# Optimization experiments

Measured on AMD Instinct MI355X. Metric: run time of the kernel, lower is better.

Reference implementation:

```python
import jax, jax.numpy as jnp
import numpy as np

NUM_HEADS = 16
D_MODEL = 1024
D_K = D_MODEL // NUM_HEADS


def setup_inputs() -> dict:
    key = jax.random.key(0)
    ks = jax.random.split(key, 11)
    B, S = 2, 2048
    s = 1.0 / np.sqrt(D_MODEL)
    return {
        "Q": jax.random.normal(ks[0], (B, S, D_MODEL), jnp.float32),
        "K": jax.random.normal(ks[1], (B, S, D_MODEL), jnp.float32),
        "V": jax.random.normal(ks[2], (B, S, D_MODEL), jnp.float32),
        "Wq": jax.random.normal(ks[3], (D_MODEL, D_MODEL), jnp.float32) * s,
        "bq": jnp.zeros((D_MODEL,), jnp.float32),
        "Wk": jax.random.normal(ks[4], (D_MODEL, D_MODEL), jnp.float32) * s,
        "bk": jnp.zeros((D_MODEL,), jnp.float32),
        "Wv": jax.random.normal(ks[5], (D_MODEL, D_MODEL), jnp.float32) * s,
        "bv": jnp.zeros((D_MODEL,), jnp.float32),
        "Wo": jax.random.normal(ks[6], (D_MODEL, D_MODEL), jnp.float32) * s,
        "bo": jnp.zeros((D_MODEL,), jnp.float32),
    }


def _split_heads(x):
    B, S, _ = x.shape
    return x.reshape(B, S, NUM_HEADS, D_K).transpose(0, 2, 1, 3)  # (B,H,S,Dk)


def reference(Q, K, V, Wq, bq, Wk, bk, Wv, bv, Wo, bo):
    q = _split_heads(Q @ Wq + bq)
    k = _split_heads(K @ Wk + bk)
    v = _split_heads(V @ Wv + bv)
    scores = jnp.einsum("bhqd,bhkd->bhqk", q, k) / jnp.sqrt(jnp.asarray(D_K, q.dtype))
    attn = jax.nn.softmax(scores, axis=-1)
    out = jnp.einsum("bhqk,bhkd->bhqd", attn, v)  # (B,H,S,Dk)
    B, H, S, Dk = out.shape
    combined = out.transpose(0, 2, 1, 3).reshape(B, S, H * Dk)
    return combined @ Wo + bo
```

## Files before the change

kernel.cpp:

```cpp
#include <hip/hip_runtime.h>
#include <stdint.h>

#define DM   1024
#define NH   16
#define DKH  64
#define SEQ  2048
#define NB   2

typedef __attribute__((ext_vector_type(8))) short  frag8;
typedef __attribute__((ext_vector_type(4))) short  frag4;
typedef __attribute__((ext_vector_type(4))) short  short4v;
typedef __attribute__((ext_vector_type(8))) short  short8v;
typedef __attribute__((ext_vector_type(4))) float  f32x4;

__device__ __forceinline__ unsigned short f2bf(float x){
  unsigned u = __float_as_uint(x);
  u += 0x7fffu + ((u >> 16) & 1u);
  return (unsigned short)(u >> 16);
}

__device__ __forceinline__ float dev_exp2(float x){
  return __builtin_amdgcn_exp2f(x);
}

#define GLOAD16(GP, LP) __builtin_amdgcn_global_load_lds( \
    (__attribute__((address_space(1))) void*)(GP), \
    (__attribute__((address_space(3))) void*)(LP), 16, 0, 0)

#define LDSFENCE() do{ asm volatile("" ::: "memory"); \
                       __builtin_amdgcn_sched_barrier(0); }while(0)


__global__ __launch_bounds__(256) void cast_qkv(const float* __restrict__ Q,
                                                const float* __restrict__ K,
                                                const float* __restrict__ V,
                                                short* __restrict__ dst){
  const int z = blockIdx.z;
  const float* src = (z == 0) ? Q : (z == 1 ? K : V);
  const int i = (blockIdx.x * 256 + threadIdx.x) * 4;
  float4 f = *(const float4*)(src + i);
  short4v s;
  s.x = (short)f2bf(f.x); s.y = (short)f2bf(f.y);
  s.z = (short)f2bf(f.z); s.w = (short)f2bf(f.w);
  *(short4v*)(dst + (long)z * (SEQ*NB*DM) + i) = s;
}

__global__ __launch_bounds__(256) void wtrans(const float* __restrict__ Wq,
                                              const float* __restrict__ Wk,
                                              const float* __restrict__ Wv,
                                              const float* __restrict__ Wo,
                                              short* __restrict__ wt){
  const int z = blockIdx.z;
  const float* W = (z == 0) ? Wq : (z == 1 ? Wk : (z == 2 ? Wv : Wo));
  short* out = wt + (long)z * (DM*DM);
  __shared__ float t[32][33];
  const int n0 = blockIdx.x * 32, k0 = blockIdx.y * 32;
  const int c = threadIdx.x & 31, r0 = threadIdx.x >> 5;
#pragma unroll
  for (int i = 0; i < 4; ++i){
    int r = r0 + i * 8;
    t[r][c] = W[(k0 + r) * DM + n0 + c];
  }
  __syncthreads();
#pragma unroll
  for (int i = 0; i < 4; ++i){
    int r = r0 + i * 8;
    out[(n0 + r) * DM + k0 + c] = (short)f2bf(t[c][r]);
  }
}

__device__ __forceinline__ void store_out(short* p, float v){ *p = (short)f2bf(v); }
__device__ __forceinline__ void store_out(float* p, float v){ *p = v; }

template<typename OT>
__global__ __launch_bounds__(256) void gemm_bt(const short* __restrict__ Abase, long Astride,
                                               const short* __restrict__ Btbase, long Btstride,
                                               const float* __restrict__ bias0,
                                               const float* __restrict__ bias1,
                                               const float* __restrict__ bias2,
                                               OT* __restrict__ Cbase, long Cstride,
                                               float qscale){
  const int z = blockIdx.z;
  const short* A  = Abase + (long)z * Astride;
  const short* Bt = Btbase + (long)z * Btstride;
  OT* C = Cbase + (long)z * Cstride;
  const float* bias = (z == 0) ? bias0 : (z == 1 ? bias1 : bias2);
  const float scale = (z == 0) ? qscale : 1.0f;
  const int KD = DM, ND = DM;

  __shared__ __align__(16) short As[128 * 64];
  __shared__ __align__(16) short Bs[128 * 64];

  const int tid = threadIdx.x;
  const int w = tid >> 6, lane = tid & 63, l15 = lane & 15, quad = lane >> 4;
  const int wy = w >> 1, wx = w & 1;
  const int bm = blockIdx.x * 128, bn = blockIdx.y * 128;
  const int lrow = lane >> 3;
  const int lcolsw = (((lane & 7) ^ lrow) & 7) * 8;

  f32x4 acc[4][4] = {};

  for (int kt = 0; kt < KD; kt += 64){
#pragma unroll
    for (int i = 0; i < 4; ++i){
      int j = w * 4 + i;
      GLOAD16(A  + (bm + j * 8 + lrow) * KD + kt + lcolsw, &As[j * 512]);
      GLOAD16(Bt + (bn + j * 8 + lrow) * KD + kt + lcolsw, &Bs[j * 512]);
    }
    __syncthreads();
#pragma unroll
    for (int ks = 0; ks < 2; ++ks){
      frag8 af[4], bf_[4];
#pragma unroll
      for (int mt = 0; mt < 4; ++mt)
        af[mt] = *(const frag8*)&As[(wy * 64 + mt * 16 + l15) * 64 +
                                    (((ks * 4 + quad) ^ (l15 & 7)) * 8)];
#pragma unroll
      for (int nt = 0; nt < 4; ++nt)
        bf_[nt] = *(const frag8*)&Bs[(wx * 64 + nt * 16 + l15) * 64 +
                                     (((ks * 4 + quad) ^ (l15 & 7)) * 8)];
#pragma unroll
      for (int mt = 0; mt < 4; ++mt)
#pragma unroll
        for (int nt = 0; nt < 4; ++nt)
          acc[mt][nt] = __builtin_amdgcn_mfma_f32_16x16x32_bf16(af[mt], bf_[nt], acc[mt][nt], 0, 0, 0);
    }
    __syncthreads();
  }

#pragma unroll
  for (int mt = 0; mt < 4; ++mt){
#pragma unroll
    for (int r = 0; r < 4; ++r){
      int m = bm + wy * 64 + mt * 16 + quad * 4 + r;
#pragma unroll
      for (int nt = 0; nt < 4; ++nt){
        int n = bn + wx * 64 + nt * 16 + l15;
        float v = (acc[mt][nt][r] + bias[n]) * scale;
        store_out(&C[(long)m * ND + n], v);
      }
    }
  }
}

template<typename OT>
__global__ __launch_bounds__(256) void gemm64_bt(const short* __restrict__ A,
                                                 const short* __restrict__ Bt,
                                                 const float* __restrict__ bias,
                                                 OT* __restrict__ C,
                                                 float scale){
  const int KD = DM, ND = DM;
  __shared__ __align__(16) short As[64 * 64];
  __shared__ __align__(16) short Bs[128 * 64];
  const int tid = threadIdx.x;
  const int w = tid >> 6, lane = tid & 63, l15 = lane & 15, quad = lane >> 4;
  const int wy = w >> 1, wx = w & 1;
  const int bm = blockIdx.x * 64, bn = blockIdx.y * 128;
  const int lrow = lane >> 3;
  const int lcolsw = (((lane & 7) ^ lrow) & 7) * 8;
  f32x4 acc[2][4] = {};

  for (int kt = 0; kt < KD; kt += 64){
#pragma unroll
    for (int i = 0; i < 2; ++i){
      int j = w * 2 + i;
      GLOAD16(A + (bm + j * 8 + lrow) * KD + kt + lcolsw, &As[j * 512]);
    }
#pragma unroll
    for (int i = 0; i < 4; ++i){
      int j = w * 4 + i;
      GLOAD16(Bt + (bn + j * 8 + lrow) * KD + kt + lcolsw, &Bs[j * 512]);
    }
    __syncthreads();
#pragma unroll
    for (int ks = 0; ks < 2; ++ks){
      frag8 af[2], bf_[4];
#pragma unroll
      for (int mt = 0; mt < 2; ++mt)
        af[mt] = *(const frag8*)&As[(wy * 32 + mt * 16 + l15) * 64 +
                                    (((ks * 4 + quad) ^ (l15 & 7)) * 8)];
#pragma unroll
      for (int nt = 0; nt < 4; ++nt)
        bf_[nt] = *(const frag8*)&Bs[(wx * 64 + nt * 16 + l15) * 64 +
                                     (((ks * 4 + quad) ^ (l15 & 7)) * 8)];
#pragma unroll
      for (int mt = 0; mt < 2; ++mt)
#pragma unroll
        for (int nt = 0; nt < 4; ++nt)
          acc[mt][nt] = __builtin_amdgcn_mfma_f32_16x16x32_bf16(af[mt], bf_[nt], acc[mt][nt], 0, 0, 0);
    }
    __syncthreads();
  }

#pragma unroll
  for (int mt = 0; mt < 2; ++mt){
#pragma unroll
    for (int r = 0; r < 4; ++r){
      int m = bm + wy * 32 + mt * 16 + quad * 4 + r;
#pragma unroll
      for (int nt = 0; nt < 4; ++nt){
        int n = bn + wx * 64 + nt * 16 + l15;
        store_out(&C[(long)m * ND + n], (acc[mt][nt][r] + bias[n]) * scale);
      }
    }
  }
}

__global__ __launch_bounds__(256) void vtrans(const short* __restrict__ v,
                                              short* __restrict__ vt){
  const int bh = blockIdx.y;
  const int b = bh >> 4, h = bh & 15;
  const int s0 = blockIdx.x * 64;
  __shared__ short tT[64][66];
  const short* vb = v + ((long)(b * SEQ + s0)) * DM + h * DKH;
  for (int j = threadIdx.x; j < 512; j += 256){
    int row = j >> 3, off = (j & 7) * 8;
    short8v d = *(const short8v*)(vb + row * DM + off);
#pragma unroll
    for (int e = 0; e < 8; ++e) tT[off + e][row] = d[e];
  }
  __syncthreads();
  short* out = vt + (long)bh * (DKH * SEQ) + s0;
  for (int j = threadIdx.x; j < 512; j += 256){
    int dr = j >> 3, soff = (j & 7) * 8;
    short8v o;
#pragma unroll
    for (int e = 0; e < 8; ++e) o[e] = tT[dr][soff + e];
    *(short8v*)(out + dr * SEQ + soff) = o;
  }
}

__global__ __launch_bounds__(256) void flash(const short* __restrict__ q,
                                             const short* __restrict__ k,
                                             const short* __restrict__ vt,
                                             short* __restrict__ comb){
  const int bh = blockIdx.y;
  const int b = bh >> 4, h = bh & 15;
  const int q0 = blockIdx.x * 128;
  const int tid = threadIdx.x;
  const int w = tid >> 6, lane = tid & 63, l15 = lane & 15, quad = lane >> 4;

  __shared__ __align__(16) short Ks[3][64 * 64];
  __shared__ __align__(16) short Vs[3][64 * 64];

  frag8 aq[2][2];
  const short* qb = q + ((long)(b * SEQ + q0 + w * 32)) * DM + h * DKH;
#pragma unroll
  for (int mt = 0; mt < 2; ++mt)
#pragma unroll
    for (int ks = 0; ks < 2; ++ks)
      aq[mt][ks] = *(const frag8*)(qb + (mt * 16 + l15) * DM + ks * 32 + quad * 8);

  frag4 ones4;
#pragma unroll
  for (int e = 0; e < 4; ++e) ones4[e] = (short)0x3F80;

  f32x4 O[2][4] = {};
  f32x4 Lacc[2] = {{0.f,0.f,0.f,0.f},{0.f,0.f,0.f,0.f}};

  const short* kb  = k + ((long)b * SEQ) * DM + h * DKH;
  const short* vtb = vt + (long)bh * (DKH * SEQ);
  const int lrow8 = lane >> 3;
  const int lcolsw = (((lane & 7) ^ lrow8) & 7) * 8;

#define STAGE(KT, BSEL) do{                                                     \
  _Pragma("unroll")                                                             \
  for (int i_ = 0; i_ < 2; ++i_){                                               \
    int jj_ = w * 2 + i_;                                                       \
    GLOAD16(kb + ((KT) * 64 + jj_ * 8 + lrow8) * DM + lcolsw,                   \
            &Ks[BSEL][jj_ * 512]);                                              \
    GLOAD16(vtb + (jj_ * 8 + lrow8) * SEQ + (KT) * 64 + lcolsw,                 \
            &Vs[BSEL][jj_ * 512]);                                              \
  } }while(0)

#define COMPUTE(BS) do{                                                         \
  __builtin_amdgcn_s_setprio(1);                                                \
  f32x4 scT[2][4];                                                              \
  _Pragma("unroll") for (int mt = 0; mt < 2; ++mt)                              \
    _Pragma("unroll") for (int nt = 0; nt < 4; ++nt)                            \
      scT[mt][nt] = (f32x4){0.f, 0.f, 0.f, 0.f};                                \
  _Pragma("unroll") for (int ks = 0; ks < 2; ++ks){                             \
    _Pragma("unroll") for (int nt = 0; nt < 4; ++nt){                           \
      frag8 ak = *(const frag8*)&Ks[BS][(nt * 16 + l15) * 64 +                  \
                                        (((ks * 4 + quad) ^ (l15 & 7)) * 8)];   \
      _Pragma("unroll") for (int mt = 0; mt < 2; ++mt)                          \
        scT[mt][nt] = __builtin_amdgcn_mfma_f32_16x16x32_bf16(                  \
            ak, aq[mt][ks], scT[mt][nt], 0, 0, 0);                              \
    }                                                                           \
  }                                                                             \
  frag4 ap[2][4];                                                               \
  _Pragma("unroll") for (int mt = 0; mt < 2; ++mt)                              \
    _Pragma("unroll") for (int nt = 0; nt < 4; ++nt){                           \
      _Pragma("unroll") for (int r = 0; r < 4; ++r){                            \
        float e = dev_exp2(scT[mt][nt][r]);                                     \
        ap[mt][nt][r] = (short)((__float_as_uint(e) + 0x8000u) >> 16);          \
      }                                                                         \
    }                                                                           \
  _Pragma("unroll") for (int nt = 0; nt < 4; ++nt){                             \
    _Pragma("unroll") for (int dt = 0; dt < 4; ++dt){                           \
      frag4 bv4 = *(const frag4*)&Vs[BS][(dt * 16 + l15) * 64 +                 \
                                   (((nt * 2 + (quad >> 1)) ^ (l15 & 7)) * 8) + \
                                   (quad & 1) * 4];                             \
      _Pragma("unroll") for (int mt = 0; mt < 2; ++mt)                          \
        O[mt][dt] = __builtin_amdgcn_mfma_f32_16x16x16bf16_1k(                  \
            ap[mt][nt], bv4, O[mt][dt], 0, 0, 0);                               \
    }                                                                           \
    _Pragma("unroll") for (int mt = 0; mt < 2; ++mt)                            \
      Lacc[mt] = __builtin_amdgcn_mfma_f32_16x16x16bf16_1k(                     \
          ap[mt][nt], ones4, Lacc[mt], 0, 0, 0);                                \
  }                                                                             \
  __builtin_amdgcn_s_setprio(0);                                                \
}while(0)

#define ITER(KT, BC, BSNEXT) do{                                                \
  STAGE((KT) + 2, BSNEXT);                                                      \
  asm volatile("s_waitcnt vmcnt(8)" ::: "memory");                              \
  __builtin_amdgcn_s_barrier();                                                 \
  LDSFENCE();                                                                   \
  COMPUTE(BC);                                                                  \
  asm volatile("s_waitcnt lgkmcnt(0)" ::: "memory");                            \
  __builtin_amdgcn_sched_barrier(0);                                            \
  __builtin_amdgcn_s_barrier();                                                 \
}while(0)

  STAGE(0, 0);
  STAGE(1, 1);
  for (int kt = 0; kt < SEQ / 64 - 2; kt += 3){
    ITER(kt,     0, 2);
    ITER(kt + 1, 1, 0);
    ITER(kt + 2, 2, 1);
  }
  asm volatile("s_waitcnt vmcnt(4)" ::: "memory");
  __builtin_amdgcn_s_barrier();
  LDSFENCE();
  COMPUTE(0);
  asm volatile("s_waitcnt vmcnt(0)" ::: "memory");
  __builtin_amdgcn_s_barrier();
  LDSFENCE();
  COMPUTE(1);

#undef ITER
#undef COMPUTE
#undef STAGE

  short* ob = comb + ((long)(b * SEQ + q0 + w * 32)) * DM + h * DKH;
#pragma unroll
  for (int mt = 0; mt < 2; ++mt){
#pragma unroll
    for (int r = 0; r < 4; ++r){
      float inv = 1.f / Lacc[mt][r];
#pragma unroll
      for (int nt = 0; nt < 4; ++nt)
        ob[(mt * 16 + quad * 4 + r) * DM + nt * 16 + l15] = (short)f2bf(O[mt][nt][r] * inv);
    }
  }
}

extern "C" void kernel_launch(void* const* d_in, const int* in_sizes, int n_in,
                              void* d_out, int out_size, void* d_ws, size_t ws_size,
                              hipStream_t stream){
  const float* Q  = (const float*)d_in[0];
  const float* K  = (const float*)d_in[1];
  const float* V  = (const float*)d_in[2];
  const float* Wq = (const float*)d_in[3];
  const float* bq = (const float*)d_in[4];
  const float* Wk = (const float*)d_in[5];
  const float* bk = (const float*)d_in[6];
  const float* Wv = (const float*)d_in[7];
  const float* bv = (const float*)d_in[8];
  const float* Wo = (const float*)d_in[9];
  const float* bo = (const float*)d_in[10];
  float* out = (float*)d_out;

  const long TEN = (long)NB * SEQ * DM;
  const long WEL = (long)DM * DM;
  short* ws   = (short*)d_ws;
  short* xc   = ws;
  short* wt   = xc + 3 * TEN;
  short* qkv  = wt + 4 * WEL;
  short* vtr  = qkv + 3 * TEN;
  short* comb = vtr + TEN;

  cast_qkv<<<dim3(4096, 1, 3), 256, 0, stream>>>(Q, K, V, xc);
  wtrans<<<dim3(32, 32, 4), 256, 0, stream>>>(Wq, Wk, Wv, Wo, wt);
  gemm_bt<short><<<dim3(32, 8, 3), 256, 0, stream>>>(xc, TEN, wt, WEL, bq, bk, bv,
                                                     qkv, TEN, 0.125f * 1.44269504f);
  vtrans<<<dim3(32, 32), 256, 0, stream>>>(qkv + 2 * TEN, vtr);
  flash<<<dim3(16, 32), 256, 0, stream>>>(qkv, qkv + TEN, vtr, comb);
  gemm64_bt<float><<<dim3(64, 8), 256, 0, stream>>>(comb, wt + 3 * WEL, bo, out, 1.0f);
  (void)in_sizes; (void)n_in; (void)out_size; (void)ws_size;
}
```

Baseline: 235.5 us.

## Double-buffer LDS tiles in projection GEMMs to overlap loads with MFMA

```diff
diff --git a/kernel.cpp b/kernel.cpp
--- a/kernel.cpp
+++ b/kernel.cpp
@@ -29,6 +29,7 @@
 
 #define LDSFENCE() do{ asm volatile("" ::: "memory"); \
                        __builtin_amdgcn_sched_barrier(0); }while(0)
+
 
 
 __global__ __launch_bounds__(256) void cast_qkv(const float* __restrict__ Q,
@@ -88,8 +89,8 @@
   const float scale = (z == 0) ? qscale : 1.0f;
   const int KD = DM, ND = DM;
 
-  __shared__ __align__(16) short As[128 * 64];
-  __shared__ __align__(16) short Bs[128 * 64];
+  __shared__ __align__(16) short As[2][128 * 64];
+  __shared__ __align__(16) short Bs[2][128 * 64];
 
   const int tid = threadIdx.x;
   const int w = tid >> 6, lane = tid & 63, l15 = lane & 15, quad = lane >> 4;
@@ -100,33 +101,49 @@
 
   f32x4 acc[4][4] = {};
 
-  for (int kt = 0; kt < KD; kt += 64){
-#pragma unroll
-    for (int i = 0; i < 4; ++i){
-      int j = w * 4 + i;
-      GLOAD16(A  + (bm + j * 8 + lrow) * KD + kt + lcolsw, &As[j * 512]);
-      GLOAD16(Bt + (bn + j * 8 + lrow) * KD + kt + lcolsw, &Bs[j * 512]);
-    }
-    __syncthreads();
-#pragma unroll
-    for (int ks = 0; ks < 2; ++ks){
-      frag8 af[4], bf_[4];
-#pragma unroll
-      for (int mt = 0; mt < 4; ++mt)
-        af[mt] = *(const frag8*)&As[(wy * 64 + mt * 16 + l15) * 64 +
-                                    (((ks * 4 + quad) ^ (l15 & 7)) * 8)];
-#pragma unroll
-      for (int nt = 0; nt < 4; ++nt)
-        bf_[nt] = *(const frag8*)&Bs[(wx * 64 + nt * 16 + l15) * 64 +
-                                     (((ks * 4 + quad) ^ (l15 & 7)) * 8)];
-#pragma unroll
-      for (int mt = 0; mt < 4; ++mt)
-#pragma unroll
-        for (int nt = 0; nt < 4; ++nt)
-          acc[mt][nt] = __builtin_amdgcn_mfma_f32_16x16x32_bf16(af[mt], bf_[nt], acc[mt][nt], 0, 0, 0);
-    }
-    __syncthreads();
-  }
+#define GSTAGE(KT, BSEL) do{                                                    \
+  _Pragma("unroll")                                                             \
+  for (int i_ = 0; i_ < 4; ++i_){                                               \
+    int j_ = w * 4 + i_;                                                        \
+    GLOAD16(A  + (bm + j_ * 8 + lrow) * KD + (KT) * 64 + lcolsw,                \
+            &As[BSEL][j_ * 512]);                                               \
+    GLOAD16(Bt + (bn + j_ * 8 + lrow) * KD + (KT) * 64 + lcolsw,                \
+            &Bs[BSEL][j_ * 512]);                                               \
+  } }while(0)
+
+#define GCOMPUTE(BS) do{                                                        \
+  _Pragma("unroll") for (int ks = 0; ks < 2; ++ks){                             \
+    frag8 af[4], bf_[4];                                                        \
+    _Pragma("unroll") for (int mt = 0; mt < 4; ++mt)                            \
+      af[mt] = *(const frag8*)&As[BS][(wy * 64 + mt * 16 + l15) * 64 +          \
+                                      (((ks * 4 + quad) ^ (l15 & 7)) * 8)];     \
+    _Pragma("unroll") for (int nt = 0; nt < 4; ++nt)                            \
+      bf_[nt] = *(const frag8*)&Bs[BS][(wx * 64 + nt * 16 + l15) * 64 +         \
+                                       (((ks * 4 + quad) ^ (l15 & 7)) * 8)];    \
+    _Pragma("unroll") for (int mt = 0; mt < 4; ++mt)                            \
+      _Pragma("unroll") for (int nt = 0; nt < 4; ++nt)                          \
+        acc[mt][nt] = __builtin_amdgcn_mfma_f32_16x16x32_bf16(                  \
+            af[mt], bf_[nt], acc[mt][nt], 0, 0, 0);                             \
+  } }while(0)
+
+  GSTAGE(0, 0);
+  for (int t = 0; t < KD / 64 - 1; ++t){
+    GSTAGE(t + 1, (t + 1) & 1);
+    asm volatile("s_waitcnt vmcnt(8)" ::: "memory");
+    __builtin_amdgcn_s_barrier();
+    LDSFENCE();
+    GCOMPUTE(t & 1);
+    asm volatile("s_waitcnt lgkmcnt(0)" ::: "memory");
+    __builtin_amdgcn_sched_barrier(0);
+    __builtin_amdgcn_s_barrier();
+  }
+  asm volatile("s_waitcnt vmcnt(0)" ::: "memory");
+  __builtin_amdgcn_s_barrier();
+  LDSFENCE();
+  GCOMPUTE(1);
+
+#undef GSTAGE
+#undef GCOMPUTE
 
 #pragma unroll
   for (int mt = 0; mt < 4; ++mt){
@@ -150,8 +167,8 @@
                                                  OT* __restrict__ C,
                                                  float scale){
   const int KD = DM, ND = DM;
-  __shared__ __align__(16) short As[64 * 64];
-  __shared__ __align__(16) short Bs[128 * 64];
+  __shared__ __align__(16) short As[2][64 * 64];
+  __shared__ __align__(16) short Bs[2][128 * 64];
   const int tid = threadIdx.x;
   const int w = tid >> 6, lane = tid & 63, l15 = lane & 15, quad = lane >> 4;
   const int wy = w >> 1, wx = w & 1;
@@ -160,37 +177,53 @@
   const int lcolsw = (((lane & 7) ^ lrow) & 7) * 8;
   f32x4 acc[2][4] = {};
 
-  for (int kt = 0; kt < KD; kt += 64){
-#pragma unroll
-    for (int i = 0; i < 2; ++i){
-      int j = w * 2 + i;
-      GLOAD16(A + (bm + j * 8 + lrow) * KD + kt + lcolsw, &As[j * 512]);
-    }
-#pragma unroll
-    for (int i = 0; i < 4; ++i){
-      int j = w * 4 + i;
-      GLOAD16(Bt + (bn + j * 8 + lrow) * KD + kt + lcolsw, &Bs[j * 512]);
-    }
-    __syncthreads();
-#pragma unroll
-    for (int ks = 0; ks < 2; ++ks){
-      frag8 af[2], bf_[4];
-#pragma unroll
-      for (int mt = 0; mt < 2; ++mt)
-        af[mt] = *(const frag8*)&As[(wy * 32 + mt * 16 + l15) * 64 +
-                                    (((ks * 4 + quad) ^ (l15 & 7)) * 8)];
-#pragma unroll
-      for (int nt = 0; nt < 4; ++nt)
-        bf_[nt] = *(const frag8*)&Bs[(wx * 64 + nt * 16 + l15) * 64 +
-                                     (((ks * 4 + quad) ^ (l15 & 7)) * 8)];
-#pragma unroll
-      for (int mt = 0; mt < 2; ++mt)
-#pragma unroll
-        for (int nt = 0; nt < 4; ++nt)
-          acc[mt][nt] = __builtin_amdgcn_mfma_f32_16x16x32_bf16(af[mt], bf_[nt], acc[mt][nt], 0, 0, 0);
-    }
-    __syncthreads();
-  }
+#define GSTAGE64(KT, BSEL) do{                                                  \
+  _Pragma("unroll")                                                             \
+  for (int i_ = 0; i_ < 2; ++i_){                                               \
+    int j_ = w * 2 + i_;                                                        \
+    GLOAD16(A + (bm + j_ * 8 + lrow) * KD + (KT) * 64 + lcolsw,                 \
+            &As[BSEL][j_ * 512]);                                               \
+  }                                                                             \
+  _Pragma("unroll")                                                             \
+  for (int i_ = 0; i_ < 4; ++i_){                                               \
+    int j_ = w * 4 + i_;                                                        \
+    GLOAD16(Bt + (bn + j_ * 8 + lrow) * KD + (KT) * 64 + lcolsw,                \
+            &Bs[BSEL][j_ * 512]);                                               \
+  } }while(0)
+
+#define GCOMPUTE64(BS) do{                                                      \
+  _Pragma("unroll") for (int ks = 0; ks < 2; ++ks){                             \
+    frag8 af[2], bf_[4];                                                        \
+    _Pragma("unroll") for (int mt = 0; mt < 2; ++mt)                            \
+      af[mt] = *(const frag8*)&As[BS][(wy * 32 + mt * 16 + l15) * 64 +          \
+                                      (((ks * 4 + quad) ^ (l15 & 7)) * 8)];     \
+    _Pragma("unroll") for (int nt = 0; nt < 4; ++nt)                            \
+      bf_[nt] = *(const frag8*)&Bs[BS][(wx * 64 + nt * 16 + l15) * 64 +         \
+                                       (((ks * 4 + quad) ^ (l15 & 7)) * 8)];    \
+    _Pragma("unroll") for (int mt = 0; mt < 2; ++mt)                            \
+      _Pragma("unroll") for (int nt = 0; nt < 4; ++nt)                          \
+        acc[mt][nt] = __builtin_amdgcn_mfma_f32_16x16x32_bf16(                  \
+            af[mt], bf_[nt], acc[mt][nt], 0, 0, 0);                             \
+  } }while(0)
+
+  GSTAGE64(0, 0);
+  for (int t = 0; t < KD / 64 - 1; ++t){
+    GSTAGE64(t + 1, (t + 1) & 1);
+    asm volatile("s_waitcnt vmcnt(6)" ::: "memory");
+    __builtin_amdgcn_s_barrier();
+    LDSFENCE();
+    GCOMPUTE64(t & 1);
+    asm volatile("s_waitcnt lgkmcnt(0)" ::: "memory");
+    __builtin_amdgcn_sched_barrier(0);
+    __builtin_amdgcn_s_barrier();
+  }
+  asm volatile("s_waitcnt vmcnt(0)" ::: "memory");
+  __builtin_amdgcn_s_barrier();
+  LDSFENCE();
+  GCOMPUTE64(1);
+
+#undef GSTAGE64
+#undef GCOMPUTE64
 
 #pragma unroll
   for (int mt = 0; mt < 2; ++mt){
```

After: 233.7 us. About the same (-0.7%).
